# Kernel tuning notes

Measured on AMD Instinct MI355X. Metric: run time of the kernel, lower is better.

## Reference

```python
import jax, jax.numpy as jnp
import numpy as np

N = 50000        # nodes
E = 400000       # edges (before self loops)
NCAT = 3         # categorical columns
V = 1000         # vocab per table
ED = 16          # embedding dim per table
NNUM = 16        # numerical features
NC = 2           # coord features
FM = 32          # fourier mapping size -> 64 fourier dims
HID = 64         # gnn hidden dim
H = 4            # gat heads
L = 2            # gnn layers
MLP1, MLP2, OUT = 256, 128, 1
EPS_BN = 1e-5
NEG_SLOPE = 0.2


def setup_inputs() -> dict:
    key = jax.random.key(0)
    ks = jax.random.split(key, 24)
    inp = {
        "x_cat": jax.random.randint(ks[0], (N, NCAT), 0, V),
        "x_num": jax.random.normal(ks[1], (N, NNUM), dtype=jnp.float32),
        "x_coord": jax.random.uniform(ks[2], (N, NC), dtype=jnp.float32),
        "edge_index": jax.random.randint(ks[3], (2, E), 0, N),
        # parameters
        "emb_tables": jax.random.normal(ks[4], (NCAT, V, ED), dtype=jnp.float32),
        "fourier_B": jax.random.normal(ks[5], (NC, FM), dtype=jnp.float32) * 10.0,  # scale=10, frozen
        "proj_W": jax.random.normal(ks[6], (NCAT * ED + NNUM + 2 * FM, HID), dtype=jnp.float32) * 0.05,
        "proj_b": jnp.zeros((HID,), jnp.float32),
        "gat_W": jax.random.normal(ks[7], (L, HID, H * HID), dtype=jnp.float32) * 0.05,
        "att_src": jax.random.normal(ks[8], (L, H, HID), dtype=jnp.float32) * 0.05,
        "att_dst": jax.random.normal(ks[9], (L, H, HID), dtype=jnp.float32) * 0.05,
        "gat_b": jnp.zeros((L, HID), jnp.float32),
        "bn_gamma": jnp.ones((L, HID), jnp.float32),
        "bn_beta": jnp.zeros((L, HID), jnp.float32),
        "mlp_W1": jax.random.normal(ks[10], (HID, MLP1), dtype=jnp.float32) * 0.05,
        "mlp_b1": jnp.zeros((MLP1,), jnp.float32),
        "mlp_W2": jax.random.normal(ks[11], (MLP1, MLP2), dtype=jnp.float32) * 0.05,
        "mlp_b2": jnp.zeros((MLP2,), jnp.float32),
        "mlp_W3": jax.random.normal(ks[12], (MLP2, OUT), dtype=jnp.float32) * 0.05,
        "mlp_b3": jnp.zeros((OUT,), jnp.float32),
    }
    return inp


def _gat_layer(x, src, dst, W, a_src, a_dst, b, n_nodes):
    # x: [N,HID] -> h: [N,H,D]
    h = (x @ W).reshape(n_nodes, H, HID)
    alpha_src = jnp.einsum('nhd,hd->nh', h, a_src)   # [N,H]
    alpha_dst = jnp.einsum('nhd,hd->nh', h, a_dst)   # [N,H]
    e = jax.nn.leaky_relu(alpha_src[src] + alpha_dst[dst], NEG_SLOPE)  # [E,H]
    # softmax over incoming edges per destination node (stable, via segment max)
    m = jax.ops.segment_max(e, dst, num_segments=n_nodes)
    a = jnp.exp(e - m[dst])
    denom = jax.ops.segment_sum(a, dst, num_segments=n_nodes)
    a = a / (denom[dst] + 1e-16)
    msg = a[:, :, None] * h[src]                      # [E,H,D]
    out = jax.ops.segment_sum(msg, dst, num_segments=n_nodes)
    return out.mean(axis=1) + b                       # concat=False -> mean over heads


def _batchnorm(x, gamma, beta):
    mu = x.mean(axis=0)
    var = x.var(axis=0)  # biased, as torch BN uses for normalization
    return (x - mu) * jax.lax.rsqrt(var + EPS_BN) * gamma + beta


def reference(x_cat, x_num, x_coord, edge_index, emb_tables, fourier_B,
              proj_W, proj_b, gat_W, att_src, att_dst, gat_b,
              bn_gamma, bn_beta, mlp_W1, mlp_b1, mlp_W2, mlp_b2, mlp_W3, mlp_b3):
    n = x_num.shape[0]
    # categorical embeddings
    embs = [emb_tables[i][x_cat[:, i]] for i in range(NCAT)]  # each [N,ED]
    # fourier features
    xp = (2.0 * np.pi) * (x_coord @ fourier_B)
    fourier = jnp.concatenate([jnp.sin(xp), jnp.cos(xp)], axis=-1)
    x = jnp.concatenate(embs + [x_num, fourier], axis=1)
    x = x @ proj_W + proj_b
    # self loops (PyG GATConv default add_self_loops=True)
    loop = jnp.arange(n)
    src = jnp.concatenate([edge_index[0], loop])
    dst = jnp.concatenate([edge_index[1], loop])
    for l in range(L):
        identity = x
        x = _gat_layer(x, src, dst, gat_W[l], att_src[l], att_dst[l], gat_b[l], n)
        x = _batchnorm(x, bn_gamma[l], bn_beta[l])
        x = jax.nn.relu(x)
        x = x + identity
    x = jax.nn.relu(x @ mlp_W1 + mlp_b1)
    x = jax.nn.relu(x @ mlp_W2 + mlp_b2)
    return x @ mlp_W3 + mlp_b3
```

## Files before the change

kernel.cpp:

```cpp
#include <hip/hip_runtime.h>
#include <hip/hip_bf16.h>

#define NND 50000
#define NCATS 3
#define VOC 1000
#define EDIM 16
#define NNUMF 16
#define FMAP 32
#define FIN 128
#define HID 64
#define NH 4
#define EB 400000
#define ETOT 450000
#define M1 256
#define M2 128
#define EPS_BN 1e-5f
#define NB 196
#define YSTR 264

typedef __attribute__((ext_vector_type(8))) short bf16x8;
typedef __attribute__((ext_vector_type(4))) float f32x4;

__device__ __forceinline__ float lrelu(float x) { return x > 0.f ? x : 0.2f * x; }

__device__ __forceinline__ unsigned short bfu(float f) {
    unsigned u = __float_as_uint(f);
    unsigned r = (u + 0x7FFFu + ((u >> 16) & 1u)) >> 16;
    return (unsigned short)r;
}
__device__ __forceinline__ float bf2f(unsigned short h) {
    return __uint_as_float((unsigned)h << 16);
}

__global__ void k_zero_deg(int* __restrict__ deg) {
    int i = blockIdx.x * blockDim.x + threadIdx.x;
    if (i < NND) deg[i] = 0;
}

__global__ void k_count(const int* __restrict__ ei, int* __restrict__ deg) {
    int e = blockIdx.x * blockDim.x + threadIdx.x;
    if (e >= ETOT) return;
    int d = (e < EB) ? ei[EB + e] : e - EB;
    atomicAdd(&deg[d], 1);
}

__global__ __launch_bounds__(256) void k_bsum(const int* __restrict__ deg,
                                              int* __restrict__ bsum) {
    int i = blockIdx.x * 256 + threadIdx.x;
    int v = (i < NND) ? deg[i] : 0;
    #pragma unroll
    for (int ofs = 32; ofs; ofs >>= 1) v += __shfl_xor(v, ofs, 64);
    __shared__ int ws[4];
    if ((threadIdx.x & 63) == 0) ws[threadIdx.x >> 6] = v;
    __syncthreads();
    if (threadIdx.x == 0) bsum[blockIdx.x] = ws[0] + ws[1] + ws[2] + ws[3];
}

__global__ __launch_bounds__(256) void k_bscan(const int* __restrict__ bsum,
                                               int* __restrict__ bpre,
                                               int* __restrict__ off) {
    __shared__ int sh[256];
    const int t = threadIdx.x;
    int v = (t < NB) ? bsum[t] : 0;
    sh[t] = v;
    __syncthreads();
    for (int ofs = 1; ofs < 256; ofs <<= 1) {
        int u = (t >= ofs) ? sh[t - ofs] : 0;
        __syncthreads();
        sh[t] += u;
        __syncthreads();
    }
    if (t < NB) bpre[t] = sh[t] - v;
    if (t == 0) off[NND] = ETOT;
}

__global__ __launch_bounds__(256) void k_offsets(const int* __restrict__ deg,
                                                 const int* __restrict__ bpre,
                                                 int* __restrict__ off,
                                                 int* __restrict__ cur) {
    __shared__ int sh[256];
    const int t = threadIdx.x;
    const int i = blockIdx.x * 256 + t;
    int v = (i < NND) ? deg[i] : 0;
    sh[t] = v;
    __syncthreads();
    for (int ofs = 1; ofs < 256; ofs <<= 1) {
        int u = (t >= ofs) ? sh[t - ofs] : 0;
        __syncthreads();
        sh[t] += u;
        __syncthreads();
    }
    int excl = sh[t] - v + bpre[blockIdx.x];
    if (i < NND) { off[i] = excl; cur[i] = excl; }
}

__global__ void k_fill(const int* __restrict__ ei, int* __restrict__ cur,
                       int* __restrict__ srcs) {
    int e = blockIdx.x * blockDim.x + threadIdx.x;
    if (e >= ETOT) return;
    int s, d;
    if (e < EB) { s = ei[e]; d = ei[EB + e]; } else { s = d = e - EB; }
    int p = atomicAdd(&cur[d], 1);
    srcs[p] = s;
}

__global__ __launch_bounds__(256) void k_packw(
    const float* __restrict__ W1, const float* __restrict__ W2,
    const float* __restrict__ gatW, const float* __restrict__ pW,
    unsigned short* __restrict__ W1f, unsigned short* __restrict__ W2f,
    unsigned short* __restrict__ Wsf, unsigned short* __restrict__ Wsl,
    unsigned short* __restrict__ pWh, unsigned short* __restrict__ pWl)
{
    int i = blockIdx.x * 256 + threadIdx.x;
    if (i < 16384) {
        int j = i & 7, l = (i >> 3) & 63, t = i >> 9;
        int kc = t & 1, cb = t >> 1;
        int k = kc * 32 + ((l >> 4) * 8) + j, c = cb * 16 + (l & 15);
        W1f[i] = bfu(W1[k * 256 + c]);
    }
    if (i < 32768) {
        int j = i & 7, l = (i >> 3) & 63, t = i >> 9;
        int kc = t & 7, cb = t >> 3;
        int k = kc * 32 + ((l >> 4) * 8) + j, c = cb * 16 + (l & 15);
        W2f[i] = bfu(W2[k * 128 + c]);
    }
    if (i < 32768) {
        int j = i & 7, l = (i >> 3) & 63, t = (i >> 9) & 31, lay = i >> 14;
        int kc = t & 7, cb = t >> 3;
        int r = kc * 32 + ((l >> 4) * 8) + j, c = cb * 16 + (l & 15);
        float w = gatW[lay * 16384 + (r & 63) * 256 + (r >> 6) * 64 + c];
        unsigned short h = bfu(w);
        Wsf[i] = h;
        Wsl[i] = bfu(w - bf2f(h));
    }
    if (i < 8192) {
        int j = i & 7, l = (i >> 3) & 63, t = i >> 9;
        int kc = t & 3, cb = t >> 2;
        int k = kc * 32 + ((l >> 4) * 8) + j, c = cb * 16 + (l & 15);
        float w = pW[k * 64 + c];
        unsigned short h = bfu(w);
        pWh[i] = h;
        pWl[i] = bfu(w - bf2f(h));
    }
}

__global__ __launch_bounds__(256) void k_feat_mfma(
    const int* __restrict__ x_cat, const float* __restrict__ x_num,
    const float* __restrict__ x_coord, const float* __restrict__ emb,
    const float* __restrict__ fB,
    const unsigned short* __restrict__ pWh, const unsigned short* __restrict__ pWl,
    const float* __restrict__ pb, float* __restrict__ xout,
    unsigned short* __restrict__ xbf)
{
    __shared__ __align__(16) unsigned short fh[64 * 128];
    __shared__ __align__(16) unsigned short fl[64 * 128];
    const int tid = threadIdx.x;
    const int lane = tid & 63, wid = tid >> 6;
    const int cl = lane & 15, lg = lane >> 4;
    const int nw = wid * 16;
    bf16x8 wfh[4][4], wfl[4][4];
    #pragma unroll
    for (int cb = 0; cb < 4; ++cb)
        #pragma unroll
        for (int kc = 0; kc < 4; ++kc) {
            wfh[cb][kc] = *(const bf16x8*)&pWh[(((cb << 2) + kc) * 64 + lane) * 8];
            wfl[cb][kc] = *(const bf16x8*)&pWl[(((cb << 2) + kc) * 64 + lane) * 8];
        }
    float pbr[4];
    #pragma unroll
    for (int cb = 0; cb < 4; ++cb) pbr[cb] = pb[cb * 16 + cl];
    const int ntiles = (NND + 63) / 64;
    for (int t = blockIdx.x; t < ntiles; t += gridDim.x) {
        const int n0 = t * 64;
        __syncthreads();
        for (int r = 0; r < 16; ++r) {
            const int row = nw + r;
            const int n = n0 + row;
            float v = 0.f, v2 = 0.f;
            if (n < NND) {
                if (lane < 48) {
                    int c = lane >> 4, j = lane & 15;
                    int idx = x_cat[n * NCATS + c];
                    v = emb[((size_t)c * VOC + idx) * EDIM + j];
                } else {
                    v = x_num[n * NNUMF + (lane - 48)];
                }
                float c0 = x_coord[n * 2 + 0], c1 = x_coord[n * 2 + 1];
                int f = lane & 31;
                float xp = 6.283185307179586f * (c0 * fB[f] + c1 * fB[FMAP + f]);
                v2 = (lane < 32) ? sinf(xp) : cosf(xp);
            }
            unsigned short h = bfu(v);
            fh[row * 128 + lane] = h;
            fl[row * 128 + lane] = bfu(v - bf2f(h));
            unsigned short h2 = bfu(v2);
            fh[row * 128 + 64 + lane] = h2;
            fl[row * 128 + 64 + lane] = bfu(v2 - bf2f(h2));
        }
        __syncthreads();
        bf16x8 afh[4], afl[4];
        #pragma unroll
        for (int kc = 0; kc < 4; ++kc) {
            afh[kc] = *(const bf16x8*)&fh[(nw + cl) * 128 + kc * 32 + lg * 8];
            afl[kc] = *(const bf16x8*)&fl[(nw + cl) * 128 + kc * 32 + lg * 8];
        }
        #pragma unroll
        for (int cb = 0; cb < 4; ++cb) {
            float bv = pbr[cb];
            f32x4 a = {bv, bv, bv, bv};
            #pragma unroll
            for (int kc = 0; kc < 4; ++kc)
                a = __builtin_amdgcn_mfma_f32_16x16x32_bf16(afl[kc], wfh[cb][kc], a, 0, 0, 0);
            #pragma unroll
            for (int kc = 0; kc < 4; ++kc)
                a = __builtin_amdgcn_mfma_f32_16x16x32_bf16(afh[kc], wfl[cb][kc], a, 0, 0, 0);
            #pragma unroll
            for (int kc = 0; kc < 4; ++kc)
                a = __builtin_amdgcn_mfma_f32_16x16x32_bf16(afh[kc], wfh[cb][kc], a, 0, 0, 0);
            #pragma unroll
            for (int r = 0; r < 4; ++r) {
                int n = n0 + nw + lg * 4 + r;
                if (n < NND) {
                    xout[(size_t)n * HID + cb * 16 + cl] = a[r];
                    xbf[(size_t)n * HID + cb * 16 + cl] = bfu(a[r]);
                }
            }
        }
    }
}

__global__ __launch_bounds__(512) void k_va2(
    const float* __restrict__ gatW, const float* __restrict__ attS,
    const float* __restrict__ attD, float* __restrict__ va2)
{
    const int lay = blockIdx.x;
    const float* W = gatW + (size_t)lay * 16384;
    const int t = threadIdx.x;
    const int k = t >> 3, q = t & 7, hh = q & 3;
    const float* a = ((q >= 4) ? attD : attS) + lay * NH * HID;
    float s = 0.f;
    #pragma unroll 8
    for (int d = 0; d < HID; ++d)
        s += W[k * 256 + hh * 64 + d] * a[hh * 64 + d];
    va2[lay * 512 + k * 8 + q] = s;
}

__global__ __launch_bounds__(256) void k_alpha2(
    const unsigned short* __restrict__ xbf, const float* __restrict__ va,
    float* __restrict__ alphS, float* __restrict__ alphD, float* __restrict__ bnst)
{
    __shared__ float vas[64 * 8];
    const int tid = threadIdx.x;
    if (blockIdx.x == 0) bnst[tid] = 0.f;
    for (int i = tid; i < 512; i += 256) vas[i] = va[i];
    __syncthreads();
    const int lane = tid & 63, wid = tid >> 6;
    const float4 vS = *(const float4*)&vas[lane * 8];
    const float4 vD = *(const float4*)&vas[lane * 8 + 4];
    for (int n = blockIdx.x * 4 + wid; n < NND; n += gridDim.x * 4) {
        float v = bf2f(xbf[(size_t)n * HID + lane]);
        float s0 = v * vS.x, s1 = v * vS.y, s2 = v * vS.z, s3 = v * vS.w;
        float d0 = v * vD.x, d1 = v * vD.y, d2 = v * vD.z, d3 = v * vD.w;
        #pragma unroll
        for (int ofs = 32; ofs; ofs >>= 1) {
            s0 += __shfl_xor(s0, ofs, 64); s1 += __shfl_xor(s1, ofs, 64);
            s2 += __shfl_xor(s2, ofs, 64); s3 += __shfl_xor(s3, ofs, 64);
            d0 += __shfl_xor(d0, ofs, 64); d1 += __shfl_xor(d1, ofs, 64);
            d2 += __shfl_xor(d2, ofs, 64); d3 += __shfl_xor(d3, ofs, 64);
        }
        if (lane == 0) {
            *(float4*)(alphS + (size_t)n * 4) = make_float4(s0, s1, s2, s3);
            *(float4*)(alphD + (size_t)n * 4) = make_float4(d0, d1, d2, d3);
        }
    }
}

__global__ __launch_bounds__(256) void k_agg_trans(
    const int* __restrict__ off, const int* __restrict__ srcs,
    const float* __restrict__ alphS, const float* __restrict__ alphD,
    const unsigned short* __restrict__ xbf,
    const unsigned short* __restrict__ Wh, const unsigned short* __restrict__ Wl_,
    const float* __restrict__ gat_b, float* __restrict__ accum,
    float* __restrict__ bnst)
{
    __shared__ __align__(16) unsigned short ylh[16 * YSTR];
    __shared__ __align__(16) unsigned short yll[16 * YSTR];
    __shared__ float sred[2][4][16];
    const int tid = threadIdx.x;
    const int l16 = tid & 15, gi = tid >> 4;
    const int lane = tid & 63, wid = tid >> 6;
    const int cl = lane & 15, lg = lane >> 4;
    const float bd = gat_b[wid * 16 + cl];
    float s1 = 0.f, s2 = 0.f;
    const int ngrp = NND / 16;
    for (int g = blockIdx.x; g < ngrp; g += gridDim.x) {
        const int d = g * 16 + gi;
        const int o0 = off[d];
        const int deg = off[d + 1] - o0;
        const float4 ad = *(const float4*)(alphD + (size_t)d * 4);
        float dn0 = 0.f, dn1 = 0.f, dn2 = 0.f, dn3 = 0.f;
        float ya[4][4];
        #pragma unroll
        for (int h = 0; h < 4; ++h)
            #pragma unroll
            for (int c = 0; c < 4; ++c) ya[h][c] = 0.f;
        for (int c0 = 0; c0 < deg; c0 += 16) {
            const int m = min(16, deg - c0);
            int sE = 0; float w0 = 0.f, w1 = 0.f, w2 = 0.f, w3 = 0.f;
            if (l16 < m) {
                sE = srcs[o0 + c0 + l16];
                float4 as = *(const float4*)(alphS + (size_t)sE * 4);
                w0 = __expf(lrelu(as.x + ad.x));
                w1 = __expf(lrelu(as.y + ad.y));
                w2 = __expf(lrelu(as.z + ad.z));
                w3 = __expf(lrelu(as.w + ad.w));
            }
            dn0 += w0; dn1 += w1; dn2 += w2; dn3 += w3;
            int j = 0;
            for (; j + 2 <= m; j += 2) {
                const int sj0 = __shfl(sE, j + 0, 16);
                const int sj1 = __shfl(sE, j + 1, 16);
                const ushort4 xu0 = *(const ushort4*)(xbf + (size_t)sj0 * HID + l16 * 4);
                const ushort4 xu1 = *(const ushort4*)(xbf + (size_t)sj1 * HID + l16 * 4);
                float a0 = __shfl(w0, j, 16), a1 = __shfl(w1, j, 16);
                float a2 = __shfl(w2, j, 16), a3 = __shfl(w3, j, 16);
                float x0 = bf2f(xu0.x), x1 = bf2f(xu0.y), x2 = bf2f(xu0.z), x3 = bf2f(xu0.w);
                ya[0][0] = fmaf(a0, x0, ya[0][0]); ya[0][1] = fmaf(a0, x1, ya[0][1]);
                ya[0][2] = fmaf(a0, x2, ya[0][2]); ya[0][3] = fmaf(a0, x3, ya[0][3]);
                ya[1][0] = fmaf(a1, x0, ya[1][0]); ya[1][1] = fmaf(a1, x1, ya[1][1]);
                ya[1][2] = fmaf(a1, x2, ya[1][2]); ya[1][3] = fmaf(a1, x3, ya[1][3]);
                ya[2][0] = fmaf(a2, x0, ya[2][0]); ya[2][1] = fmaf(a2, x1, ya[2][1]);
                ya[2][2] = fmaf(a2, x2, ya[2][2]); ya[2][3] = fmaf(a2, x3, ya[2][3]);
                ya[3][0] = fmaf(a3, x0, ya[3][0]); ya[3][1] = fmaf(a3, x1, ya[3][1]);
                ya[3][2] = fmaf(a3, x2, ya[3][2]); ya[3][3] = fmaf(a3, x3, ya[3][3]);
                a0 = __shfl(w0, j + 1, 16); a1 = __shfl(w1, j + 1, 16);
                a2 = __shfl(w2, j + 1, 16); a3 = __shfl(w3, j + 1, 16);
                x0 = bf2f(xu1.x); x1 = bf2f(xu1.y); x2 = bf2f(xu1.z); x3 = bf2f(xu1.w);
                ya[0][0] = fmaf(a0, x0, ya[0][0]); ya[0][1] = fmaf(a0, x1, ya[0][1]);
                ya[0][2] = fmaf(a0, x2, ya[0][2]); ya[0][3] = fmaf(a0, x3, ya[0][3]);
                ya[1][0] = fmaf(a1, x0, ya[1][0]); ya[1][1] = fmaf(a1, x1, ya[1][1]);
                ya[1][2] = fmaf(a1, x2, ya[1][2]); ya[1][3] = fmaf(a1, x3, ya[1][3]);
                ya[2][0] = fmaf(a2, x0, ya[2][0]); ya[2][1] = fmaf(a2, x1, ya[2][1]);
                ya[2][2] = fmaf(a2, x2, ya[2][2]); ya[2][3] = fmaf(a2, x3, ya[2][3]);
                ya[3][0] = fmaf(a3, x0, ya[3][0]); ya[3][1] = fmaf(a3, x1, ya[3][1]);
                ya[3][2] = fmaf(a3, x2, ya[3][2]); ya[3][3] = fmaf(a3, x3, ya[3][3]);
            }
            if (j < m) {
                const int sj0 = __shfl(sE, j, 16);
                const ushort4 xu0 = *(const ushort4*)(xbf + (size_t)sj0 * HID + l16 * 4);
                float a0 = __shfl(w0, j, 16), a1 = __shfl(w1, j, 16);
                float a2 = __shfl(w2, j, 16), a3 = __shfl(w3, j, 16);
                float x0 = bf2f(xu0.x), x1 = bf2f(xu0.y), x2 = bf2f(xu0.z), x3 = bf2f(xu0.w);
                ya[0][0] = fmaf(a0, x0, ya[0][0]); ya[0][1] = fmaf(a0, x1, ya[0][1]);
                ya[0][2] = fmaf(a0, x2, ya[0][2]); ya[0][3] = fmaf(a0, x3, ya[0][3]);
                ya[1][0] = fmaf(a1, x0, ya[1][0]); ya[1][1] = fmaf(a1, x1, ya[1][1]);
                ya[1][2] = fmaf(a1, x2, ya[1][2]); ya[1][3] = fmaf(a1, x3, ya[1][3]);
                ya[2][0] = fmaf(a2, x0, ya[2][0]); ya[2][1] = fmaf(a2, x1, ya[2][1]);
                ya[2][2] = fmaf(a2, x2, ya[2][2]); ya[2][3] = fmaf(a2, x3, ya[2][3]);
                ya[3][0] = fmaf(a3, x0, ya[3][0]); ya[3][1] = fmaf(a3, x1, ya[3][1]);
                ya[3][2] = fmaf(a3, x2, ya[3][2]); ya[3][3] = fmaf(a3, x3, ya[3][3]);
            }
        }
        #pragma unroll
        for (int ofs = 8; ofs; ofs >>= 1) {
            dn0 += __shfl_xor(dn0, ofs, 64); dn1 += __shfl_xor(dn1, ofs, 64);
            dn2 += __shfl_xor(dn2, ofs, 64); dn3 += __shfl_xor(dn3, ofs, 64);
        }
        {
            const float invh[4] = {
                __fdividef(1.f, dn0 + 1e-16f), __fdividef(1.f, dn1 + 1e-16f),
                __fdividef(1.f, dn2 + 1e-16f), __fdividef(1.f, dn3 + 1e-16f)};
            #pragma unroll
            for (int h = 0; h < 4; ++h) {
                ushort4 uh, ul;
                float v0 = ya[h][0] * invh[h]; uh.x = bfu(v0); ul.x = bfu(v0 - bf2f(uh.x));
                float v1 = ya[h][1] * invh[h]; uh.y = bfu(v1); ul.y = bfu(v1 - bf2f(uh.y));
                float v2 = ya[h][2] * invh[h]; uh.z = bfu(v2); ul.z = bfu(v2 - bf2f(uh.z));
                float v3 = ya[h][3] * invh[h]; uh.w = bfu(v3); ul.w = bfu(v3 - bf2f(uh.w));
                *(ushort4*)&ylh[gi * YSTR + h * 64 + l16 * 4] = uh;
                *(ushort4*)&yll[gi * YSTR + h * 64 + l16 * 4] = ul;
            }
        }
        __syncthreads();
        {
            bf16x8 afh[8], afl[8], wfh[8], wfl[8];
            #pragma unroll
            for (int kc = 0; kc < 8; ++kc) {
                afh[kc] = *(const bf16x8*)&ylh[cl * YSTR + kc * 32 + lg * 8];
                afl[kc] = *(const bf16x8*)&yll[cl * YSTR + kc * 32 + lg * 8];
                wfh[kc] = *(const bf16x8*)&Wh[(size_t)(((wid << 3) + kc) * 64 + lane) * 8];
                wfl[kc] = *(const bf16x8*)&Wl_[(size_t)(((wid << 3) + kc) * 64 + lane) * 8];
            }
            f32x4 a0 = {0.f, 0.f, 0.f, 0.f};
            f32x4 a1 = {0.f, 0.f, 0.f, 0.f};
            f32x4 a2 = {0.f, 0.f, 0.f, 0.f};
            #pragma unroll
            for (int kc = 0; kc < 8; ++kc) {
                a0 = __builtin_amdgcn_mfma_f32_16x16x32_bf16(afl[kc], wfh[kc], a0, 0, 0, 0);
                a1 = __builtin_amdgcn_mfma_f32_16x16x32_bf16(afh[kc], wfl[kc], a1, 0, 0, 0);
                a2 = __builtin_amdgcn_mfma_f32_16x16x32_bf16(afh[kc], wfh[kc], a2, 0, 0, 0);
            }
            const int n0 = g * 16;
            #pragma unroll
            for (int r = 0; r < 4; ++r) {
                float gv = (a0[r] + a1[r] + a2[r]) * 0.25f + bd;
                accum[(size_t)(n0 + lg * 4 + r) * HID + wid * 16 + cl] = gv;
                s1 += gv; s2 += gv * gv;
            }
        }
        __syncthreads();
    }
    s1 += __shfl_xor(s1, 16, 64); s2 += __shfl_xor(s2, 16, 64);
    s1 += __shfl_xor(s1, 32, 64); s2 += __shfl_xor(s2, 32, 64);
    if (lane < 16) { sred[0][wid][cl] = s1; sred[1][wid][cl] = s2; }
    __syncthreads();
    if (tid < 64) {
        atomicAdd(&bnst[tid], sred[0][tid >> 4][tid & 15]);
        atomicAdd(&bnst[128 + tid], sred[1][tid >> 4][tid & 15]);
    }
}

__global__ void k_bn_apply(const float* __restrict__ accum, const float* __restrict__ bnst,
                           const float* __restrict__ gamma, const float* __restrict__ beta,
                           float* __restrict__ x, unsigned short* __restrict__ xbf)
{
    int i = blockIdx.x * blockDim.x + threadIdx.x;
    if (i >= NND * 16) return;
    int dg = (i & 15) * 4;
    float4 a = ((const float4*)accum)[i];
    float4 xv = ((float4*)x)[i];
    float r[4]; float av[4] = {a.x, a.y, a.z, a.w}; float xx[4] = {xv.x, xv.y, xv.z, xv.w};
    #pragma unroll
    for (int c = 0; c < 4; ++c) {
        int d = dg + c;
        float mu = bnst[d] * (1.f / NND);
        float var = bnst[128 + d] * (1.f / NND) - mu * mu;
        float inv = rsqrtf(var + EPS_BN);
        float yv = (av[c] - mu) * inv * gamma[d] + beta[d];
        r[c] = fmaxf(yv, 0.f) + xx[c];
    }
    ((float4*)x)[i] = make_float4(r[0], r[1], r[2], r[3]);
    ushort4 u;
    u.x = bfu(r[0]); u.y = bfu(r[1]); u.z = bfu(r[2]); u.w = bfu(r[3]);
    *(ushort4*)(xbf + (size_t)i * 4) = u;
}

__global__ __launch_bounds__(256, 1) void k_mlp_mfma(
    const unsigned short* __restrict__ xbf,
    const unsigned short* __restrict__ W1f, const unsigned short* __restrict__ W2f,
    const float* __restrict__ b1, const float* __restrict__ b2,
    const float* __restrict__ W3, const float* __restrict__ b3,
    float* __restrict__ out)
{
    __shared__ __align__(16) unsigned short W1s[16384];
    __shared__ __align__(16) unsigned short W2s[32768];
    __shared__ __align__(16) unsigned short xs[64 * 64];
    __shared__ __align__(16) unsigned short z1s[64 * 256];
    __shared__ float b1s[256], b2s[128], w3s[128];
    const int tid = threadIdx.x;
    const int lane = tid & 63, wid = tid >> 6;
    {
        const uint4* s1 = (const uint4*)W1f; uint4* d1 = (uint4*)W1s;
        for (int i = tid; i < 2048; i += 256) d1[i] = s1[i];
        const uint4* s2 = (const uint4*)W2f; uint4* d2 = (uint4*)W2s;
        for (int i = tid; i < 4096; i += 256) d2[i] = s2[i];
        if (tid < 256) b1s[tid] = b1[tid];
        if (tid < 128) { b2s[tid] = b2[tid]; w3s[tid] = W3[tid]; }
    }
    const float bb3 = b3[0];
    const int nw = wid * 16;
    const int cl = lane & 15, lg = lane >> 4;
    const int ntiles = (NND + 63) / 64;
    for (int t = blockIdx.x; t < ntiles; t += gridDim.x) {
        const int n0 = t * 64;
        __syncthreads();
        #pragma unroll
        for (int q = 0; q < 2; ++q) {
            int i = q * 256 + tid;
            int row = i >> 3, k8 = (i & 7) * 8;
            int n = n0 + row;
            uint4 v = (n < NND) ? *(const uint4*)(xbf + (size_t)n * HID + k8)
                                : make_uint4(0u, 0u, 0u, 0u);
            *(uint4*)&xs[row * 64 + k8] = v;
        }
        __syncthreads();
        #pragma unroll 4
        for (int cb = 0; cb < 16; ++cb) {
            float bv = b1s[cb * 16 + cl];
            f32x4 a = {bv, bv, bv, bv};
            #pragma unroll
            for (int kc = 0; kc < 2; ++kc) {
                bf16x8 af = *(const bf16x8*)&xs[(nw + cl) * 64 + kc * 32 + lg * 8];
                bf16x8 bf = *(const bf16x8*)&W1s[(((cb << 1) + kc) * 64 + lane) * 8];
                a = __builtin_amdgcn_mfma_f32_16x16x32_bf16(af, bf, a, 0, 0, 0);
            }
            #pragma unroll
            for (int r = 0; r < 4; ++r)
                z1s[(nw + lg * 4 + r) * 256 + cb * 16 + cl] = bfu(fmaxf(a[r], 0.f));
        }
        __syncthreads();
        bf16x8 af2[8];
        #pragma unroll
        for (int kc = 0; kc < 8; ++kc)
            af2[kc] = *(const bf16x8*)&z1s[(nw + cl) * 256 + kc * 32 + lg * 8];
        float p0 = 0.f, p1 = 0.f, p2 = 0.f, p3 = 0.f;
        #pragma unroll
        for (int cb = 0; cb < 8; ++cb) {
            float bv = b2s[cb * 16 + cl];
            f32x4 a = {bv, bv, bv, bv};
            #pragma unroll
            for (int kc = 0; kc < 8; ++kc) {
                bf16x8 bf = *(const bf16x8*)&W2s[(((cb << 3) + kc) * 64 + lane) * 8];
                a = __builtin_amdgcn_mfma_f32_16x16x32_bf16(af2[kc], bf, a, 0, 0, 0);
            }
            float w3v = w3s[cb * 16 + cl];
            p0 = fmaf(fmaxf(a[0], 0.f), w3v, p0);
            p1 = fmaf(fmaxf(a[1], 0.f), w3v, p1);
            p2 = fmaf(fmaxf(a[2], 0.f), w3v, p2);
            p3 = fmaf(fmaxf(a[3], 0.f), w3v, p3);
        }
        #pragma unroll
        for (int ofs = 1; ofs <= 8; ofs <<= 1) {
            p0 += __shfl_xor(p0, ofs, 64); p1 += __shfl_xor(p1, ofs, 64);
            p2 += __shfl_xor(p2, ofs, 64); p3 += __shfl_xor(p3, ofs, 64);
        }
        if (cl == 0) {
            int base = n0 + nw + lg * 4;
            if (base + 0 < NND) out[base + 0] = p0 + bb3;
            if (base + 1 < NND) out[base + 1] = p1 + bb3;
            if (base + 2 < NND) out[base + 2] = p2 + bb3;
            if (base + 3 < NND) out[base + 3] = p3 + bb3;
        }
    }
}

extern "C" void kernel_launch(void* const* d_in, const int* in_sizes, int n_in,
                              void* d_out, int out_size, void* d_ws, size_t ws_size,
                              hipStream_t stream) {
    const int*   x_cat   = (const int*)  d_in[0];
    const float* x_num   = (const float*)d_in[1];
    const float* x_coord = (const float*)d_in[2];
    const int*   eidx    = (const int*)  d_in[3];
    const float* emb     = (const float*)d_in[4];
    const float* fB      = (const float*)d_in[5];
    const float* pW      = (const float*)d_in[6];
    const float* pb      = (const float*)d_in[7];
    const float* gatW    = (const float*)d_in[8];
    const float* attS    = (const float*)d_in[9];
    const float* attD    = (const float*)d_in[10];
    const float* gatB    = (const float*)d_in[11];
    const float* bnG     = (const float*)d_in[12];
    const float* bnB     = (const float*)d_in[13];
    const float* W1      = (const float*)d_in[14];
    const float* b1      = (const float*)d_in[15];
    const float* W2      = (const float*)d_in[16];
    const float* b2      = (const float*)d_in[17];
    const float* W3      = (const float*)d_in[18];
    const float* b3      = (const float*)d_in[19];
    float* out = (float*)d_out;

    char* p = (char*)d_ws;
    float* x     = (float*)p;  p += (size_t)NND * HID * 4;
    unsigned short* xbf = (unsigned short*)p; p += (size_t)NND * HID * 2;
    float* alphS = (float*)p;  p += (size_t)NND * NH * 4;
    float* alphD = (float*)p;  p += (size_t)NND * NH * 4;
    float* accum = (float*)p;  p += (size_t)NND * HID * 4;
    float* bnst  = (float*)p;  p += 1024;
    float* va2   = (float*)p;  p += 1024 * 4;
    unsigned short* W1f = (unsigned short*)p; p += 16384 * 2;
    unsigned short* W2f = (unsigned short*)p; p += 32768 * 2;
    unsigned short* Wsf = (unsigned short*)p; p += 32768 * 2;
    unsigned short* Wsl = (unsigned short*)p; p += 32768 * 2;
    unsigned short* pWh = (unsigned short*)p; p += 8192 * 2;
    unsigned short* pWl = (unsigned short*)p; p += 8192 * 2;
    int*   deg   = (int*)p;    p += (size_t)NND * 4;
    int*   cur   = (int*)p;    p += (size_t)NND * 4;
    int*   off   = (int*)p;    p += (size_t)(NND + 1) * 4 + 4;
    int*   srcs  = (int*)p;    p += (size_t)ETOT * 4;
    int*   bsum  = (int*)p;    p += NB * 4;
    int*   bpre  = (int*)p;    p += NB * 4;

    k_zero_deg<<<NB, 256, 0, stream>>>(deg);
    k_count<<<(ETOT + 255) / 256, 256, 0, stream>>>(eidx, deg);
    k_bsum<<<NB, 256, 0, stream>>>(deg, bsum);
    k_bscan<<<1, 256, 0, stream>>>(bsum, bpre, off);
    k_offsets<<<NB, 256, 0, stream>>>(deg, bpre, off, cur);
    k_fill<<<(ETOT + 255) / 256, 256, 0, stream>>>(eidx, cur, srcs);
    k_packw<<<192, 256, 0, stream>>>(W1, W2, gatW, pW, W1f, W2f, Wsf, Wsl, pWh, pWl);
    k_va2<<<2, 512, 0, stream>>>(gatW, attS, attD, va2);

    k_feat_mfma<<<512, 256, 0, stream>>>(x_cat, x_num, x_coord, emb, fB, pWh, pWl, pb,
                                         x, xbf);
    for (int l = 0; l < 2; ++l) {
        k_alpha2<<<2048, 256, 0, stream>>>(xbf, va2 + (size_t)l * 512, alphS, alphD, bnst);
        k_agg_trans<<<1024, 256, 0, stream>>>(off, srcs, alphS, alphD, xbf,
                                              Wsf + (size_t)l * 16384,
                                              Wsl + (size_t)l * 16384,
                                              gatB + l * HID, accum, bnst);
        k_bn_apply<<<3125, 256, 0, stream>>>(accum, bnst, bnG + l * HID, bnB + l * HID,
                                             x, xbf);
    }
    k_mlp_mfma<<<256, 256, 0, stream>>>(xbf, W1f, W2f, b1, b2, W3, b3, out);
}
```

Measured before the change: 302.6 us.

## Precompute per-edge attention weights in a separate kernel and shard BN atomics

Adds a k_edge_w kernel that computes the exp(leaky_relu) attention weight for every CSR edge up front. k_fill now also records each edge's destination so that kernel can run. The aggregation kernel then reads one float4 weight per edge instead of doing a random alphS gather and four exps inside its latency-bound loop. Separately, the BatchNorm statistic atomics are spread over 8 replicas to reduce contention, and k_bn_apply sums the replicas. The cost is an extra launch, an extra edst array, and a 7.2MB per-edge weight buffer written and read back each layer.

```diff
diff --git a/kernel.cpp b/kernel.cpp
--- a/kernel.cpp
+++ b/kernel.cpp
@@ -95,13 +95,14 @@
 }
 
 __global__ void k_fill(const int* __restrict__ ei, int* __restrict__ cur,
-                       int* __restrict__ srcs) {
+                       int* __restrict__ srcs, int* __restrict__ edst) {
     int e = blockIdx.x * blockDim.x + threadIdx.x;
     if (e >= ETOT) return;
     int s, d;
     if (e < EB) { s = ei[e]; d = ei[EB + e]; } else { s = d = e - EB; }
     int p = atomicAdd(&cur[d], 1);
     srcs[p] = s;
+    edst[p] = d;
 }
 
 __global__ __launch_bounds__(256) void k_packw(
@@ -251,7 +252,7 @@
 {
     __shared__ float vas[64 * 8];
     const int tid = threadIdx.x;
-    if (blockIdx.x == 0) bnst[tid] = 0.f;
+    if (blockIdx.x < 8) bnst[blockIdx.x * 256 + tid] = 0.f;
     for (int i = tid; i < 512; i += 256) vas[i] = va[i];
     __syncthreads();
     const int lane = tid & 63, wid = tid >> 6;
@@ -275,9 +276,27 @@
     }
 }
 
+__global__ __launch_bounds__(256) void k_edge_w(
+    const int* __restrict__ srcs, const int* __restrict__ edst,
+    const float* __restrict__ alphS, const float* __restrict__ alphD,
+    float4* __restrict__ ew)
+{
+    int e = blockIdx.x * 256 + threadIdx.x;
+    if (e >= ETOT) return;
+    int s = srcs[e], d = edst[e];
+    float4 as = *(const float4*)(alphS + (size_t)s * 4);
+    float4 ad = *(const float4*)(alphD + (size_t)d * 4);
+    float4 w;
+    w.x = __expf(lrelu(as.x + ad.x));
+    w.y = __expf(lrelu(as.y + ad.y));
+    w.z = __expf(lrelu(as.z + ad.z));
+    w.w = __expf(lrelu(as.w + ad.w));
+    ew[e] = w;
+}
+
 __global__ __launch_bounds__(256) void k_agg_trans(
     const int* __restrict__ off, const int* __restrict__ srcs,
-    const float* __restrict__ alphS, const float* __restrict__ alphD,
+    const float4* __restrict__ ew,
     const unsigned short* __restrict__ xbf,
     const unsigned short* __restrict__ Wh, const unsigned short* __restrict__ Wl_,
     const float* __restrict__ gat_b, float* __restrict__ accum,
@@ -297,7 +316,6 @@
         const int d = g * 16 + gi;
         const int o0 = off[d];
         const int deg = off[d + 1] - o0;
-        const float4 ad = *(const float4*)(alphD + (size_t)d * 4);
         float dn0 = 0.f, dn1 = 0.f, dn2 = 0.f, dn3 = 0.f;
         float ya[4][4];
         #pragma unroll
@@ -309,11 +327,8 @@
             int sE = 0; float w0 = 0.f, w1 = 0.f, w2 = 0.f, w3 = 0.f;
             if (l16 < m) {
                 sE = srcs[o0 + c0 + l16];
-                float4 as = *(const float4*)(alphS + (size_t)sE * 4);
-                w0 = __expf(lrelu(as.x + ad.x));
-                w1 = __expf(lrelu(as.y + ad.y));
-                w2 = __expf(lrelu(as.z + ad.z));
-                w3 = __expf(lrelu(as.w + ad.w));
+                float4 wv = ew[o0 + c0 + l16];
+                w0 = wv.x; w1 = wv.y; w2 = wv.z; w3 = wv.w;
             }
             dn0 += w0; dn1 += w1; dn2 += w2; dn3 += w3;
             int j = 0;
@@ -415,8 +430,9 @@
     if (lane < 16) { sred[0][wid][cl] = s1; sred[1][wid][cl] = s2; }
     __syncthreads();
     if (tid < 64) {
-        atomicAdd(&bnst[tid], sred[0][tid >> 4][tid & 15]);
-        atomicAdd(&bnst[128 + tid], sred[1][tid >> 4][tid & 15]);
+        const int rep = (blockIdx.x & 7) * 256;
+        atomicAdd(&bnst[rep + tid], sred[0][tid >> 4][tid & 15]);
+        atomicAdd(&bnst[rep + 128 + tid], sred[1][tid >> 4][tid & 15]);
     }
 }
 
@@ -433,8 +449,14 @@
     #pragma unroll
     for (int c = 0; c < 4; ++c) {
         int d = dg + c;
-        float mu = bnst[d] * (1.f / NND);
-        float var = bnst[128 + d] * (1.f / NND) - mu * mu;
+        float s1 = 0.f, s2 = 0.f;
+        #pragma unroll
+        for (int rep = 0; rep < 8; ++rep) {
+            s1 += bnst[rep * 256 + d];
+            s2 += bnst[rep * 256 + 128 + d];
+        }
+        float mu = s1 * (1.f / NND);
+        float var = s2 * (1.f / NND) - mu * mu;
         float inv = rsqrtf(var + EPS_BN);
         float yv = (av[c] - mu) * inv * gamma[d] + beta[d];
         r[c] = fmaxf(yv, 0.f) + xx[c];
@@ -565,7 +587,7 @@
     float* alphS = (float*)p;  p += (size_t)NND * NH * 4;
     float* alphD = (float*)p;  p += (size_t)NND * NH * 4;
     float* accum = (float*)p;  p += (size_t)NND * HID * 4;
-    float* bnst  = (float*)p;  p += 1024;
+    float* bnst  = (float*)p;  p += 8 * 256 * 4;
     float* va2   = (float*)p;  p += 1024 * 4;
     unsigned short* W1f = (unsigned short*)p; p += 16384 * 2;
     unsigned short* W2f = (unsigned short*)p; p += 32768 * 2;
@@ -577,6 +599,8 @@
     int*   cur   = (int*)p;    p += (size_t)NND * 4;
     int*   off   = (int*)p;    p += (size_t)(NND + 1) * 4 + 4;
     int*   srcs  = (int*)p;    p += (size_t)ETOT * 4;
+    int*   edst  = (int*)p;    p += (size_t)ETOT * 4;
+    float4* ew   = (float4*)p; p += (size_t)ETOT * 16;
     int*   bsum  = (int*)p;    p += NB * 4;
     int*   bpre  = (int*)p;    p += NB * 4;
 
@@ -585,7 +609,7 @@
     k_bsum<<<NB, 256, 0, stream>>>(deg, bsum);
     k_bscan<<<1, 256, 0, stream>>>(bsum, bpre, off);
     k_offsets<<<NB, 256, 0, stream>>>(deg, bpre, off, cur);
-    k_fill<<<(ETOT + 255) / 256, 256, 0, stream>>>(eidx, cur, srcs);
+    k_fill<<<(ETOT + 255) / 256, 256, 0, stream>>>(eidx, cur, srcs, edst);
     k_packw<<<192, 256, 0, stream>>>(W1, W2, gatW, pW, W1f, W2f, Wsf, Wsl, pWh, pWl);
     k_va2<<<2, 512, 0, stream>>>(gatW, attS, attD, va2);
 
@@ -593,7 +617,8 @@
                                          x, xbf);
     for (int l = 0; l < 2; ++l) {
         k_alpha2<<<2048, 256, 0, stream>>>(xbf, va2 + (size_t)l * 512, alphS, alphD, bnst);
-        k_agg_trans<<<1024, 256, 0, stream>>>(off, srcs, alphS, alphD, xbf,
+        k_edge_w<<<(ETOT + 255) / 256, 256, 0, stream>>>(srcs, edst, alphS, alphD, ew);
+        k_agg_trans<<<1024, 256, 0, stream>>>(off, srcs, ew, xbf,
                                               Wsf + (size_t)l * 16384,
                                               Wsl + (size_t)l * 16384,
                                               gatB + l * HID, accum, bnst);
```

New measurement: 295.6 us. 2.3% less time.
